# Optimization experiments

Measured on AMD Instinct MI355X. Metric: run time of the kernel, lower is better.

## Reference

```python
import jax, jax.numpy as jnp
import numpy as np

N_HEADS = 16
COS_SIM_SCALE = 8.0  # lucidrains flash_cosine_sim_attention default temperature
RMS_EPS = 1e-6
ROPE_THETA = 10000.0


def _rms_norm(t, g):
    # RMSNorm over head dim with learnable gain (QKNorm)
    return t * jax.lax.rsqrt(jnp.mean(t * t, axis=-1, keepdims=True) + RMS_EPS) * g


def _rotate_half(x):
    d = x.shape[-1]
    return jnp.concatenate([-x[..., d // 2:], x[..., : d // 2]], axis=-1)


def _image_rope_cos_sin(n, d, dtype):
    # 2D axial RoPE: first half of head dim encodes row position, second half column.
    side = int(np.sqrt(n))
    assert side * side == n, 'ImageRoPE expects a square token grid'
    n_freq = d // 4
    freqs = 1.0 / (ROPE_THETA ** (jnp.arange(n_freq, dtype=jnp.float32) / n_freq))
    pos = jnp.arange(side, dtype=jnp.float32)
    grid_h = jnp.repeat(pos, side)   # (n,) row index
    grid_w = jnp.tile(pos, side)     # (n,) col index
    ang_h = grid_h[:, None] * freqs  # (n, d//4)
    ang_w = grid_w[:, None] * freqs  # (n, d//4)
    # rotate-half convention: angles for dims [0:d//2] paired with [d//2:d]
    ang = jnp.concatenate([ang_h, ang_w], axis=-1)          # (n, d//2)
    ang = jnp.concatenate([ang, ang], axis=-1)              # (n, d)
    return jnp.cos(ang).astype(dtype), jnp.sin(ang).astype(dtype)


def setup_inputs() -> dict:
    key = jax.random.key(0)
    ks = jax.random.split(key, 6)
    b, n, dm = 8, 1024, 1024
    h = N_HEADS
    d = dm // h
    s = 1.0 / np.sqrt(dm)
    return {
        'x': jax.random.normal(ks[0], (b, n, dm), dtype=jnp.float32),
        'w_qkv': jax.random.normal(ks[1], (dm, 3 * dm), dtype=jnp.float32) * s,
        'b_qkv': jnp.zeros((3 * dm,), dtype=jnp.float32),
        'q_gain': jnp.ones((d,), dtype=jnp.float32),
        'k_gain': jnp.ones((d,), dtype=jnp.float32),
        'w_out': jax.random.normal(ks[2], (dm, dm), dtype=jnp.float32) * s,
        'b_out': jnp.zeros((dm,), dtype=jnp.float32),
    }


def reference(x, w_qkv, b_qkv, q_gain, k_gain, w_out, b_out):
    b, n, dm = x.shape
    h = N_HEADS
    d = dm // h
    qkv = x @ w_qkv + b_qkv                       # (b, n, 3*dm)
    qkv = qkv.reshape(b, n, 3, h, d)
    qkv = jnp.transpose(qkv, (2, 0, 3, 1, 4))     # (3, b, h, n, d)
    q, k, v = qkv[0], qkv[1], qkv[2]
    # QK-norm (RMSNorm over head dim)
    q = _rms_norm(q, q_gain)
    k = _rms_norm(k, k_gain)
    # 2D image RoPE
    cos, sin = _image_rope_cos_sin(n, d, x.dtype)
    q = q * cos + _rotate_half(q) * sin
    k = k * cos + _rotate_half(k) * sin
    # cosine-sim attention: l2-normalize q,k, fixed scale, softmax, weighted sum
    q = q / jnp.linalg.norm(q, axis=-1, keepdims=True)
    k = k / jnp.linalg.norm(k, axis=-1, keepdims=True)
    scores = jnp.einsum('bhnd,bhmd->bhnm', q, k) * COS_SIM_SCALE
    attn = jax.nn.softmax(scores, axis=-1)
    o = jnp.einsum('bhnm,bhmd->bhnd', attn, v)    # (b, h, n, d)
    o = jnp.transpose(o, (0, 2, 1, 3)).reshape(b, n, dm)
    return o @ w_out + b_out
```

## Files before the change

kernel.cpp:

```cpp
#include <hip/hip_runtime.h>
#include <hip/hip_bf16.h>
#include <cstdint>

typedef __bf16 bf16;
typedef __bf16 bf16x8 __attribute__((ext_vector_type(8)));
typedef __bf16 bf16x4 __attribute__((ext_vector_type(4)));
typedef float f32x4 __attribute__((ext_vector_type(4)));

__device__ inline bf16x8 cvt8(const float* __restrict__ p) {
  float4 a = *(const float4*)p;
  float4 b = *(const float4*)(p + 4);
  bf16x8 r;
  r[0] = (bf16)a.x; r[1] = (bf16)a.y; r[2] = (bf16)a.z; r[3] = (bf16)a.w;
  r[4] = (bf16)b.x; r[5] = (bf16)b.y; r[6] = (bf16)b.z; r[7] = (bf16)b.w;
  return r;
}

__device__ inline void gl_lds16(const bf16* g, bf16* l) {
  auto gp = reinterpret_cast<const __attribute__((address_space(1))) uint32_t*>(
      reinterpret_cast<uintptr_t>(g));
  auto lp = reinterpret_cast<__attribute__((address_space(3))) uint32_t*>(
      reinterpret_cast<uintptr_t>(l));
  __builtin_amdgcn_global_load_lds(gp, lp, 16, 0, 0);
}

__global__ __launch_bounds__(256) void cast_k(const float* __restrict__ in,
                                              bf16* __restrict__ out) {
  long i = ((long)blockIdx.x * 256 + threadIdx.x) * 8;
  *(bf16x8*)(out + i) = cvt8(in + i);
}

__global__ __launch_bounds__(256) void transpose_cast_k(const float* __restrict__ in,
                                                        bf16* __restrict__ out,
                                                        int R, int C) {
  __shared__ bf16 T[32][33];
  int tc = blockIdx.x * 32, tr = blockIdx.y * 32;
  int c = threadIdx.x & 31, r8 = threadIdx.x >> 5;
#pragma unroll
  for (int i = 0; i < 4; i++) {
    int r = r8 + i * 8;
    T[r][c] = (bf16)in[(long)(tr + r) * C + tc + c];
  }
  __syncthreads();
#pragma unroll
  for (int i = 0; i < 4; i++) {
    int r = r8 + i * 8;
    out[(long)(tc + r) * R + tr + c] = T[c][r];
  }
}

template <int EPI>
__global__ __launch_bounds__(256, 5) void gemm_bt(const bf16* __restrict__ A,
                                                  const bf16* __restrict__ Bt,
                                                  const float* __restrict__ bias,
                                                  int M, int N, int K,
                                                  float* __restrict__ out,
                                                  bf16* __restrict__ qb,
                                                  bf16* __restrict__ kb,
                                                  bf16* __restrict__ v4,
                                                  const float* __restrict__ qg,
                                                  const float* __restrict__ kg) {
  __shared__ __align__(16) bf16 As[128][32];
  __shared__ __align__(16) bf16 Bs[128][32];

  const int tid = threadIdx.x;
  const int lane = tid & 63;
  const int w = tid >> 6;
  const int wm = (w & 1) * 64;
  const int wn = (w >> 1) * 64;
  const int quad = lane >> 4;
  const int l16 = lane & 15;

  const int m0 = blockIdx.y * 128;
  const int n0 = blockIdx.x * 128;

  const int sr = w * 32 + (lane >> 2);
  const int sc = (lane & 3) * 8;

  f32x4 acc[4][4];
#pragma unroll
  for (int i = 0; i < 4; i++)
#pragma unroll
    for (int j = 0; j < 4; j++) acc[i][j] = f32x4{0.f, 0.f, 0.f, 0.f};

  for (int k0 = 0; k0 < K; k0 += 32) {
    __syncthreads();
    const bf16 *ga0, *ga1;
    if (EPI == 0) {
      ga0 = A + (long)(m0 + sr) * K + k0 + sc;
      ga1 = ga0 + (long)16 * K;
    } else {
      int hh = k0 >> 6, dc = (k0 & 63) + sc;
      int m1 = m0 + sr, m2 = m1 + 16;
      ga0 = A + ((long)((m1 >> 10) * 16 + hh) * 1024 + (m1 & 1023)) * 64 + dc;
      ga1 = A + ((long)((m2 >> 10) * 16 + hh) * 1024 + (m2 & 1023)) * 64 + dc;
    }
    gl_lds16(ga0, &As[w * 32][0]);
    gl_lds16(ga1, &As[w * 32 + 16][0]);
    gl_lds16(Bt + (long)(n0 + sr) * K + k0 + sc, &Bs[w * 32][0]);
    gl_lds16(Bt + (long)(n0 + sr + 16) * K + k0 + sc, &Bs[w * 32 + 16][0]);
    __syncthreads();

    bf16x8 af[4], bfr[4];
#pragma unroll
    for (int i = 0; i < 4; i++) {
      af[i] = *(const bf16x8*)&As[wm + i * 16 + l16][quad * 8];
      bfr[i] = *(const bf16x8*)&Bs[wn + i * 16 + l16][quad * 8];
    }
#pragma unroll
    for (int i = 0; i < 4; i++)
#pragma unroll
      for (int j = 0; j < 4; j++)
        acc[i][j] = __builtin_amdgcn_mfma_f32_16x16x32_bf16(af[i], bfr[j], acc[i][j], 0, 0, 0);
  }

  if (EPI == 1) {
#pragma unroll
    for (int i = 0; i < 4; i++)
#pragma unroll
      for (int j = 0; j < 4; j++)
#pragma unroll
        for (int r = 0; r < 4; r++) {
          int mg = m0 + wm + i * 16 + quad * 4 + r;
          int ng = n0 + wn + j * 16 + l16;
          out[(long)mg * N + ng] = acc[i][j][r] + bias[ng];
        }
    return;
  }

  const int which = n0 >> 10;
  if (which == 2) {
    const int T0 = (((m0 & 1023) + wm) >> 2) + quad;
#pragma unroll
    for (int i = 0; i < 4; i++) {
#pragma unroll
      for (int j = 0; j < 4; j++) {
        int ng = n0 + wn + j * 16 + l16;
        int rem = ng & 1023, head = rem >> 6, dc = rem & 63;
        int bh = (m0 >> 10) * 16 + head;
        float bj = bias[ng];
        bf16x4 pv;
#pragma unroll
        for (int r = 0; r < 4; r++) pv[r] = (bf16)(acc[i][j][r] + bj);
        *(bf16x4*)(v4 + ((long)bh * 16384 + (long)(T0 + i * 4) * 64 + dc) * 4) = pv;
      }
    }
    return;
  }

  const float* gg = which ? kg : qg;
  bf16* dst = which ? kb : qb;
  const float fold = which ? 1.0f : 8.0f;
  const int h = ((n0 + wn) & 1023) >> 6;
  const int bh = (m0 >> 10) * 16 + h;
  float bj[4], gain[4];
#pragma unroll
  for (int j = 0; j < 4; j++) {
    bj[j] = bias[n0 + wn + j * 16 + l16];
    gain[j] = gg[j * 16 + l16];
  }
  const float f = exp2f((float)l16 * (-13.287712379549449f / 16.0f));

#pragma unroll
  for (int i = 0; i < 4; i++) {
#pragma unroll
    for (int r = 0; r < 4; r++) {
      int ntok = (m0 & 1023) + wm + i * 16 + quad * 4 + r;
      float v0 = acc[i][0][r] + bj[0];
      float v1 = acc[i][1][r] + bj[1];
      float v2 = acc[i][2][r] + bj[2];
      float v3 = acc[i][3][r] + bj[3];
      float ss = v0 * v0 + v1 * v1 + v2 * v2 + v3 * v3;
#pragma unroll
      for (int m = 1; m <= 8; m <<= 1) ss += __shfl_xor(ss, m, 64);
      float rms = rsqrtf(ss * (1.0f / 64.0f) + 1e-6f);
      v0 *= rms * gain[0]; v1 *= rms * gain[1]; v2 *= rms * gain[2]; v3 *= rms * gain[3];
      float sh, ch_, swv, cw;
      __sincosf((float)(ntok >> 5) * f, &sh, &ch_);
      __sincosf((float)(ntok & 31) * f, &swv, &cw);
      float w0 = v0 * ch_ - v2 * sh;
      float w1 = v1 * cw - v3 * swv;
      float w2 = v2 * ch_ + v0 * sh;
      float w3 = v3 * cw + v1 * swv;
      float nn = w0 * w0 + w1 * w1 + w2 * w2 + w3 * w3;
#pragma unroll
      for (int m = 1; m <= 8; m <<= 1) nn += __shfl_xor(nn, m, 64);
      float inv = rsqrtf(nn) * fold;
      long base = ((long)bh * 1024 + ntok) * 64 + l16;
      dst[base] = (bf16)(w0 * inv);
      dst[base + 16] = (bf16)(w1 * inv);
      dst[base + 32] = (bf16)(w2 * inv);
      dst[base + 48] = (bf16)(w3 * inv);
    }
  }
}

__global__ __launch_bounds__(256, 2) void attn_k(bf16* __restrict__ qb,
                                                 const bf16* __restrict__ kb,
                                                 const bf16* __restrict__ v4) {
  __shared__ __align__(16) bf16 Ks[64][72];
  __shared__ __align__(16) bf16 Vl[4096];
  __shared__ __align__(16) bf16 Ps[4][16][72];

  const int tid = threadIdx.x;
  const int lane = tid & 63;
  const int w = tid >> 6;
  const int quad = lane >> 4;
  const int l16 = lane & 15;

  const int bh = blockIdx.y;
  const int q0 = blockIdx.x * 256 + w * 64;

  bf16x8 aq[4][2];
  long qrow[4];
#pragma unroll
  for (int g = 0; g < 4; g++) {
    qrow[g] = ((long)bh * 1024 + q0 + g * 16 + l16) * 64;
    aq[g][0] = *(const bf16x8*)(qb + qrow[g] + quad * 8);
    aq[g][1] = *(const bf16x8*)(qb + qrow[g] + 32 + quad * 8);
  }

  f32x4 o[4][4];
#pragma unroll
  for (int g = 0; g < 4; g++)
#pragma unroll
    for (int i = 0; i < 4; i++) o[g][i] = f32x4{0.f, 0.f, 0.f, 0.f};
  float ls[4] = {0.f, 0.f, 0.f, 0.f};

  const int sr = tid >> 3, sc = (tid & 7) * 8;
  const bf16* kbase = kb + (long)bh * 65536;
  const bf16* vbase = v4 + (long)bh * 65536;

  for (int kt = 0; kt < 1024; kt += 64) {
    __syncthreads();
    *(bf16x8*)&Ks[sr][sc]      = *(const bf16x8*)(kbase + (long)(kt + sr) * 64 + sc);
    *(bf16x8*)&Ks[sr + 32][sc] = *(const bf16x8*)(kbase + (long)(kt + sr + 32) * 64 + sc);
    gl_lds16(vbase + (long)kt * 64 + (w * 2) * 512 + lane * 8, &Vl[(w * 2) * 512]);
    gl_lds16(vbase + (long)kt * 64 + (w * 2 + 1) * 512 + lane * 8, &Vl[(w * 2 + 1) * 512]);
    __syncthreads();

    bf16x8 kf[4][2], vf[4][2];
#pragma unroll
    for (int i = 0; i < 4; i++) {
      kf[i][0] = *(const bf16x8*)&Ks[i * 16 + l16][quad * 8];
      kf[i][1] = *(const bf16x8*)&Ks[i * 16 + l16][32 + quad * 8];
      int D4 = (i * 16 + l16) * 4;
      bf16x4 a0 = *(const bf16x4*)&Vl[quad * 512 + D4];
      bf16x4 a1 = *(const bf16x4*)&Vl[quad * 512 + D4 + 256];
      bf16x4 a2 = *(const bf16x4*)&Vl[quad * 512 + D4 + 2048];
      bf16x4 a3 = *(const bf16x4*)&Vl[quad * 512 + D4 + 2048 + 256];
      vf[i][0] = __builtin_shufflevector(a0, a1, 0, 1, 2, 3, 4, 5, 6, 7);
      vf[i][1] = __builtin_shufflevector(a2, a3, 0, 1, 2, 3, 4, 5, 6, 7);
    }

#pragma unroll
    for (int g = 0; g < 4; g++) {
#pragma unroll
      for (int i = 0; i < 4; i++) {
        f32x4 st = f32x4{0.f, 0.f, 0.f, 0.f};
        st = __builtin_amdgcn_mfma_f32_16x16x32_bf16(kf[i][0], aq[g][0], st, 0, 0, 0);
        st = __builtin_amdgcn_mfma_f32_16x16x32_bf16(kf[i][1], aq[g][1], st, 0, 0, 0);
        bf16x4 pk;
#pragma unroll
        for (int r = 0; r < 4; r++) {
          float p = __expf(st[r] - 8.0f);
          ls[g] += p;
          pk[r] = (bf16)p;
        }
        *(bf16x4*)&Ps[w][l16][i * 16 + quad * 4] = pk;
      }
      asm volatile("s_waitcnt lgkmcnt(0)" ::: "memory");
      bf16x8 bp0 = *(const bf16x8*)&Ps[w][l16][quad * 8];
      bf16x8 bp1 = *(const bf16x8*)&Ps[w][l16][32 + quad * 8];
#pragma unroll
      for (int i = 0; i < 4; i++) {
        o[g][i] = __builtin_amdgcn_mfma_f32_16x16x32_bf16(vf[i][0], bp0, o[g][i], 0, 0, 0);
        o[g][i] = __builtin_amdgcn_mfma_f32_16x16x32_bf16(vf[i][1], bp1, o[g][i], 0, 0, 0);
      }
    }
  }

#pragma unroll
  for (int g = 0; g < 4; g++) {
    float l = ls[g];
    l += __shfl_xor(l, 16, 64);
    l += __shfl_xor(l, 32, 64);
    float inv = 1.0f / l;
#pragma unroll
    for (int i = 0; i < 4; i++) {
      bf16x4 ov;
#pragma unroll
      for (int r = 0; r < 4; r++) ov[r] = (bf16)(o[g][i][r] * inv);
      *(bf16x4*)(qb + qrow[g] + i * 16 + quad * 4) = ov;
    }
  }
}

extern "C" void kernel_launch(void* const* d_in, const int* in_sizes, int n_in,
                              void* d_out, int out_size, void* d_ws, size_t ws_size,
                              hipStream_t stream) {
  (void)in_sizes; (void)n_in; (void)out_size; (void)ws_size;
  const float* x     = (const float*)d_in[0];
  const float* w_qkv = (const float*)d_in[1];
  const float* b_qkv = (const float*)d_in[2];
  const float* q_g   = (const float*)d_in[3];
  const float* k_g   = (const float*)d_in[4];
  const float* w_out = (const float*)d_in[5];
  const float* b_out = (const float*)d_in[6];
  float* out = (float*)d_out;

  char* ws = (char*)d_ws;
  bf16* wqkvT = (bf16*)ws; ws += (long)3072 * 1024 * 2;
  bf16* woT   = (bf16*)ws; ws += (long)1024 * 1024 * 2;
  bf16* xb    = (bf16*)ws; ws += (long)8192 * 1024 * 2;
  bf16* qb    = (bf16*)ws; ws += (long)128 * 1024 * 64 * 2;
  bf16* kb    = (bf16*)ws; ws += (long)128 * 1024 * 64 * 2;
  bf16* v4    = (bf16*)ws; ws += (long)128 * 64 * 1024 * 2;

  cast_k<<<4096, 256, 0, stream>>>(x, xb);
  transpose_cast_k<<<dim3(3072 / 32, 1024 / 32), 256, 0, stream>>>(w_qkv, wqkvT, 1024, 3072);
  transpose_cast_k<<<dim3(1024 / 32, 1024 / 32), 256, 0, stream>>>(w_out, woT, 1024, 1024);
  gemm_bt<0><<<dim3(3072 / 128, 8192 / 128), 256, 0, stream>>>(xb, wqkvT, b_qkv,
                                                               8192, 3072, 1024,
                                                               (float*)nullptr, qb, kb, v4,
                                                               q_g, k_g);
  attn_k<<<dim3(4, 128), 256, 0, stream>>>(qb, kb, v4);
  gemm_bt<1><<<dim3(1024 / 128, 8192 / 128), 256, 0, stream>>>(qb, woT, b_out,
                                                               8192, 1024, 1024,
                                                               out, (bf16*)nullptr,
                                                               (bf16*)nullptr, (bf16*)nullptr,
                                                               (const float*)nullptr,
                                                               (const float*)nullptr);
}
```

Measured before the change: 292.1 us.

## Replace GEMM with 256x256 double-buffered swizzled LDS tile pipeline

Replaces the 128x128 single-buffered GEMM with a 512-thread, 256x256-tile kernel using BK=64. It double-buffers LDS with staged async global-to-LDS loads interleaved between MFMA phases, uses an XOR swizzle to avoid LDS bank conflicts, remaps blocks for L2 locality and raises MFMA wave priority. The goal is to hide global load latency and raise data reuse per tile. The cost is higher register and LDS use (128KB of LDS, 32 accumulators per thread), many barriers, and fewer blocks for the small output GEMM (128 blocks).

```diff
diff --git a/kernel.cpp b/kernel.cpp
--- a/kernel.cpp
+++ b/kernel.cpp
@@ -49,8 +49,10 @@
   }
 }
 
+#define BAR() asm volatile("s_barrier" ::: "memory")
+
 template <int EPI>
-__global__ __launch_bounds__(256, 5) void gemm_bt(const bf16* __restrict__ A,
+__global__ __launch_bounds__(512, 2) void gemm256(const bf16* __restrict__ A,
                                                   const bf16* __restrict__ Bt,
                                                   const float* __restrict__ bias,
                                                   int M, int N, int K,
@@ -60,89 +62,151 @@
                                                   bf16* __restrict__ v4,
                                                   const float* __restrict__ qg,
                                                   const float* __restrict__ kg) {
-  __shared__ __align__(16) bf16 As[128][32];
-  __shared__ __align__(16) bf16 Bs[128][32];
+  __shared__ __align__(16) bf16 As[2][16384];
+  __shared__ __align__(16) bf16 Bs[2][16384];
 
   const int tid = threadIdx.x;
   const int lane = tid & 63;
   const int w = tid >> 6;
-  const int wm = (w & 1) * 64;
-  const int wn = (w >> 1) * 64;
   const int quad = lane >> 4;
   const int l16 = lane & 15;
-
-  const int m0 = blockIdx.y * 128;
-  const int n0 = blockIdx.x * 128;
-
-  const int sr = w * 32 + (lane >> 2);
-  const int sc = (lane & 3) * 8;
-
-  f32x4 acc[4][4];
-#pragma unroll
-  for (int i = 0; i < 4; i++)
+  const int wr = w >> 2;
+  const int wc = w & 3;
+
+  const int gx = gridDim.x;
+  const int bid = blockIdx.y * gx + blockIdx.x;
+  const int cpx = (gx * gridDim.y) >> 3;
+  const int sw = (bid & 7) * cpx + (bid >> 3);
+  const int n0 = (sw % gx) * 256;
+  const int m0 = (sw / gx) * 256;
+
+  int srow[2], scof[2];
+#pragma unroll
+  for (int l = 0; l < 2; l++) {
+    int s = l * 512 + tid;
+    srow[l] = s >> 3;
+    scof[l] = ((s & 7) ^ ((s >> 3) & 7)) * 8;
+  }
+  const bf16 *aB0, *aB1;
+  if (EPI == 0) {
+    aB0 = A + (long)(m0 + srow[0]) * K + scof[0];
+    aB1 = A + (long)(m0 + srow[1]) * K + scof[1];
+  } else {
+    aB0 = A + (long)(m0 >> 10) * 1048576 + (long)((m0 & 1023) + srow[0]) * 64 + scof[0];
+    aB1 = A + (long)(m0 >> 10) * 1048576 + (long)((m0 & 1023) + srow[1]) * 64 + scof[1];
+  }
+  const bf16* bB0 = Bt + (long)(n0 + srow[0]) * K + scof[0];
+  const bf16* bB1 = Bt + (long)(n0 + srow[1]) * K + scof[1];
+
+#define STAGE_A(tb, kt1, h)                                                       \
+  {                                                                               \
+    const bf16* g0 = (EPI == 0) ? (aB0 + (long)(h)*128 * K + (kt1)*64)            \
+                                : (aB0 + (long)(h)*8192 + (long)(kt1)*65536);     \
+    const bf16* g1 = (EPI == 0) ? (aB1 + (long)(h)*128 * K + (kt1)*64)            \
+                                : (aB1 + (long)(h)*8192 + (long)(kt1)*65536);     \
+    gl_lds16(g0, &As[tb][(h)*8192 + w * 512]);                                    \
+    gl_lds16(g1, &As[tb][(h)*8192 + 4096 + w * 512]);                             \
+  }
+#define STAGE_B(tb, kt1, h)                                                       \
+  {                                                                               \
+    gl_lds16(bB0 + (long)(h)*128 * K + (kt1)*64, &Bs[tb][(h)*8192 + w * 512]);    \
+    gl_lds16(bB1 + (long)(h)*128 * K + (kt1)*64,                                  \
+             &Bs[tb][(h)*8192 + 4096 + w * 512]);                                 \
+  }
+
+  const int cq0 = ((quad) ^ (l16 & 7)) * 8;
+  const int cq1 = ((4 + quad) ^ (l16 & 7)) * 8;
+  const int aoff = wr * 8192 + l16 * 64;
+  const int boff = wc * 4096 + l16 * 64;
+
+  f32x4 acc[8][4];
+#pragma unroll
+  for (int i = 0; i < 8; i++)
 #pragma unroll
     for (int j = 0; j < 4; j++) acc[i][j] = f32x4{0.f, 0.f, 0.f, 0.f};
 
-  for (int k0 = 0; k0 < K; k0 += 32) {
-    __syncthreads();
-    const bf16 *ga0, *ga1;
-    if (EPI == 0) {
-      ga0 = A + (long)(m0 + sr) * K + k0 + sc;
-      ga1 = ga0 + (long)16 * K;
+#define MM16(MLO, AF, BF)                                                         \
+  __builtin_amdgcn_s_setprio(1);                                                  \
+  _Pragma("unroll") for (int mm = 0; mm < 4; mm++)                                \
+      _Pragma("unroll") for (int nn = 0; nn < 4; nn++) acc[(MLO) + mm][nn] =      \
+          __builtin_amdgcn_mfma_f32_16x16x32_bf16(AF[mm], BF[nn],                 \
+                                                  acc[(MLO) + mm][nn], 0, 0, 0);  \
+  __builtin_amdgcn_s_setprio(0);
+
+  const int NK = K >> 6;
+  STAGE_A(0, 0, 0); STAGE_A(0, 0, 1); STAGE_B(0, 0, 0); STAGE_B(0, 0, 1);
+
+  for (int kt = 0; kt < NK; ++kt) {
+    const int pb = kt & 1;
+    const int tb = pb ^ 1;
+    const bool pf = (kt + 1 < NK);
+    bf16x8 afr[4], bfr[4];
+    if (pf) {
+      STAGE_A(tb, kt + 1, 0);
+      asm volatile("s_waitcnt vmcnt(2)" ::: "memory");
     } else {
-      int hh = k0 >> 6, dc = (k0 & 63) + sc;
-      int m1 = m0 + sr, m2 = m1 + 16;
-      ga0 = A + ((long)((m1 >> 10) * 16 + hh) * 1024 + (m1 & 1023)) * 64 + dc;
-      ga1 = A + ((long)((m2 >> 10) * 16 + hh) * 1024 + (m2 & 1023)) * 64 + dc;
-    }
-    gl_lds16(ga0, &As[w * 32][0]);
-    gl_lds16(ga1, &As[w * 32 + 16][0]);
-    gl_lds16(Bt + (long)(n0 + sr) * K + k0 + sc, &Bs[w * 32][0]);
-    gl_lds16(Bt + (long)(n0 + sr + 16) * K + k0 + sc, &Bs[w * 32 + 16][0]);
-    __syncthreads();
-
-    bf16x8 af[4], bfr[4];
-#pragma unroll
-    for (int i = 0; i < 4; i++) {
-      af[i] = *(const bf16x8*)&As[wm + i * 16 + l16][quad * 8];
-      bfr[i] = *(const bf16x8*)&Bs[wn + i * 16 + l16][quad * 8];
-    }
-#pragma unroll
-    for (int i = 0; i < 4; i++)
-#pragma unroll
-      for (int j = 0; j < 4; j++)
-        acc[i][j] = __builtin_amdgcn_mfma_f32_16x16x32_bf16(af[i], bfr[j], acc[i][j], 0, 0, 0);
+      asm volatile("s_waitcnt vmcnt(0)" ::: "memory");
+    }
+    BAR();
+#pragma unroll
+    for (int n = 0; n < 4; n++) bfr[n] = *(const bf16x8*)&Bs[pb][boff + n * 1024 + cq0];
+#pragma unroll
+    for (int m = 0; m < 4; m++) afr[m] = *(const bf16x8*)&As[pb][aoff + m * 1024 + cq0];
+    MM16(0, afr, bfr)
+    BAR();
+#pragma unroll
+    for (int m = 0; m < 4; m++)
+      afr[m] = *(const bf16x8*)&As[pb][aoff + 4096 + m * 1024 + cq0];
+    if (pf) STAGE_A(tb, kt + 1, 1);
+    BAR();
+    MM16(4, afr, bfr)
+    BAR();
+#pragma unroll
+    for (int n = 0; n < 4; n++) bfr[n] = *(const bf16x8*)&Bs[pb][boff + n * 1024 + cq1];
+#pragma unroll
+    for (int m = 0; m < 4; m++) afr[m] = *(const bf16x8*)&As[pb][aoff + m * 1024 + cq1];
+    if (pf) STAGE_B(tb, kt + 1, 0);
+    BAR();
+    MM16(0, afr, bfr)
+    BAR();
+#pragma unroll
+    for (int m = 0; m < 4; m++)
+      afr[m] = *(const bf16x8*)&As[pb][aoff + 4096 + m * 1024 + cq1];
+    if (pf) STAGE_B(tb, kt + 1, 1);
+    BAR();
+    MM16(4, afr, bfr)
+    BAR();
   }
 
   if (EPI == 1) {
 #pragma unroll
-    for (int i = 0; i < 4; i++)
-#pragma unroll
-      for (int j = 0; j < 4; j++)
+    for (int m = 0; m < 8; m++)
+#pragma unroll
+      for (int n = 0; n < 4; n++)
 #pragma unroll
         for (int r = 0; r < 4; r++) {
-          int mg = m0 + wm + i * 16 + quad * 4 + r;
-          int ng = n0 + wn + j * 16 + l16;
-          out[(long)mg * N + ng] = acc[i][j][r] + bias[ng];
+          int mg = m0 + wr * 128 + m * 16 + quad * 4 + r;
+          int ng = n0 + wc * 64 + n * 16 + l16;
+          out[(long)mg * N + ng] = acc[m][n][r] + bias[ng];
         }
     return;
   }
 
   const int which = n0 >> 10;
   if (which == 2) {
-    const int T0 = (((m0 & 1023) + wm) >> 2) + quad;
-#pragma unroll
-    for (int i = 0; i < 4; i++) {
-#pragma unroll
-      for (int j = 0; j < 4; j++) {
-        int ng = n0 + wn + j * 16 + l16;
-        int rem = ng & 1023, head = rem >> 6, dc = rem & 63;
-        int bh = (m0 >> 10) * 16 + head;
+    const int T0 = (((m0 & 1023) + wr * 128) >> 2) + quad;
+    const int bh = (m0 >> 10) * 16 + ((n0 & 1023) >> 6) + wc;
+#pragma unroll
+    for (int m = 0; m < 8; m++) {
+#pragma unroll
+      for (int n = 0; n < 4; n++) {
+        int ng = n0 + wc * 64 + n * 16 + l16;
+        int dc = n * 16 + l16;
         float bj = bias[ng];
         bf16x4 pv;
 #pragma unroll
-        for (int r = 0; r < 4; r++) pv[r] = (bf16)(acc[i][j][r] + bj);
-        *(bf16x4*)(v4 + ((long)bh * 16384 + (long)(T0 + i * 4) * 64 + dc) * 4) = pv;
+        for (int r = 0; r < 4; r++) pv[r] = (bf16)(acc[m][n][r] + bj);
+        *(bf16x4*)(v4 + ((long)bh * 16384 + (long)(T0 + m * 4) * 64 + dc) * 4) = pv;
       }
     }
     return;
@@ -151,28 +215,28 @@
   const float* gg = which ? kg : qg;
   bf16* dst = which ? kb : qb;
   const float fold = which ? 1.0f : 8.0f;
-  const int h = ((n0 + wn) & 1023) >> 6;
+  const int h = ((n0 + wc * 64) & 1023) >> 6;
   const int bh = (m0 >> 10) * 16 + h;
   float bj[4], gain[4];
 #pragma unroll
   for (int j = 0; j < 4; j++) {
-    bj[j] = bias[n0 + wn + j * 16 + l16];
+    bj[j] = bias[n0 + wc * 64 + j * 16 + l16];
     gain[j] = gg[j * 16 + l16];
   }
   const float f = exp2f((float)l16 * (-13.287712379549449f / 16.0f));
 
 #pragma unroll
-  for (int i = 0; i < 4; i++) {
+  for (int m = 0; m < 8; m++) {
 #pragma unroll
     for (int r = 0; r < 4; r++) {
-      int ntok = (m0 & 1023) + wm + i * 16 + quad * 4 + r;
-      float v0 = acc[i][0][r] + bj[0];
-      float v1 = acc[i][1][r] + bj[1];
-      float v2 = acc[i][2][r] + bj[2];
-      float v3 = acc[i][3][r] + bj[3];
+      int ntok = (m0 & 1023) + wr * 128 + m * 16 + quad * 4 + r;
+      float v0 = acc[m][0][r] + bj[0];
+      float v1 = acc[m][1][r] + bj[1];
+      float v2 = acc[m][2][r] + bj[2];
+      float v3 = acc[m][3][r] + bj[3];
       float ss = v0 * v0 + v1 * v1 + v2 * v2 + v3 * v3;
 #pragma unroll
-      for (int m = 1; m <= 8; m <<= 1) ss += __shfl_xor(ss, m, 64);
+      for (int mk = 1; mk <= 8; mk <<= 1) ss += __shfl_xor(ss, mk, 64);
       float rms = rsqrtf(ss * (1.0f / 64.0f) + 1e-6f);
       v0 *= rms * gain[0]; v1 *= rms * gain[1]; v2 *= rms * gain[2]; v3 *= rms * gain[3];
       float sh, ch_, swv, cw;
@@ -184,7 +248,7 @@
       float w3 = v3 * cw + v1 * swv;
       float nn = w0 * w0 + w1 * w1 + w2 * w2 + w3 * w3;
 #pragma unroll
-      for (int m = 1; m <= 8; m <<= 1) nn += __shfl_xor(nn, m, 64);
+      for (int mk = 1; mk <= 8; mk <<= 1) nn += __shfl_xor(nn, mk, 64);
       float inv = rsqrtf(nn) * fold;
       long base = ((long)bh * 1024 + ntok) * 64 + l16;
       dst[base] = (bf16)(w0 * inv);
@@ -320,12 +384,12 @@
   cast_k<<<4096, 256, 0, stream>>>(x, xb);
   transpose_cast_k<<<dim3(3072 / 32, 1024 / 32), 256, 0, stream>>>(w_qkv, wqkvT, 1024, 3072);
   transpose_cast_k<<<dim3(1024 / 32, 1024 / 32), 256, 0, stream>>>(w_out, woT, 1024, 1024);
-  gemm_bt<0><<<dim3(3072 / 128, 8192 / 128), 256, 0, stream>>>(xb, wqkvT, b_qkv,
+  gemm256<0><<<dim3(3072 / 256, 8192 / 256), 512, 0, stream>>>(xb, wqkvT, b_qkv,
                                                                8192, 3072, 1024,
                                                                (float*)nullptr, qb, kb, v4,
                                                                q_g, k_g);
   attn_k<<<dim3(4, 128), 256, 0, stream>>>(qb, kb, v4);
-  gemm_bt<1><<<dim3(1024 / 128, 8192 / 128), 256, 0, stream>>>(qb, woT, b_out,
+  gemm256<1><<<dim3(1024 / 256, 8192 / 256), 512, 0, stream>>>(qb, woT, b_out,
                                                                8192, 1024, 1024,
                                                                out, (bf16*)nullptr,
                                                                (bf16*)nullptr, (bf16*)nullptr,
```

Result: faster. 264.9 us (-9.3%).
